# Performance work log

Measured on AMD Instinct MI355X. Metric: run time of the kernel, lower is better.

## Reference

```python
import jax, jax.numpy as jnp
import numpy as np

N_NODES = 100000
N_EDGES = 3200000
IN_DIM = 256
HIDDEN = 128
OUT_DIM = 64


def setup_inputs() -> dict:
    key = jax.random.key(0)
    k = jax.random.split(key, 6)
    x = jax.random.normal(k[0], (N_NODES, IN_DIM), dtype=jnp.float32)
    adj_vals = jax.random.uniform(k[1], (N_EDGES,), dtype=jnp.float32)
    # glorot init as in the original
    s1 = np.sqrt(6.0 / (IN_DIM + HIDDEN)).astype(np.float32)
    s2 = np.sqrt(6.0 / (HIDDEN + OUT_DIM)).astype(np.float32)
    w1 = jax.random.uniform(k[2], (IN_DIM, HIDDEN), dtype=jnp.float32, minval=-s1, maxval=s1)
    w2 = jax.random.uniform(k[3], (HIDDEN, OUT_DIM), dtype=jnp.float32, minval=-s2, maxval=s2)
    edge_src = jax.random.randint(k[4], (N_EDGES,), 0, N_NODES, dtype=jnp.int32)
    edge_dst = jax.random.randint(k[5], (N_EDGES,), 0, N_NODES, dtype=jnp.int32)
    return {"x": x, "adj_vals": adj_vals, "w1": w1, "w2": w2,
            "edge_src": edge_src, "edge_dst": edge_dst}


def _spmm(adj_vals, edge_src, edge_dst, h, n_nodes):
    """Sparse adjacency (COO) times dense matrix: out[d] = sum_e vals[e]*h[src[e]]."""
    msgs = adj_vals[:, None] * h[edge_src]  # [E, D] gather + scale
    return jax.ops.segment_sum(msgs, edge_dst, num_segments=n_nodes)


def reference(x, adj_vals, w1, w2, edge_src, edge_dst):
    # Layer 1: pre_sup = X @ W1; support = A @ pre_sup; relu
    h = jax.nn.relu(_spmm(adj_vals, edge_src, edge_dst, x @ w1, N_NODES))
    # Layer 2: identity activation -> logits
    logits = _spmm(adj_vals, edge_src, edge_dst, h @ w2, N_NODES)
    return logits
```

## Files before the change

kernel.cpp:

```cpp
#include <hip/hip_runtime.h>

#define N_NODES 100000
#define N_EDGES 3200000
#define IN_DIM 256
#define HIDDEN 128
#define OUT_DIM 64

#define NBUCK 782
#define CHUNK 2560
#define NPT (CHUNK / 256)
#define BCAP 6144
#define CURSTRIDE 32

typedef unsigned int uint32;
typedef unsigned short ushort16;

typedef short short8 __attribute__((ext_vector_type(8)));
typedef float f32x4 __attribute__((ext_vector_type(4)));

__device__ __forceinline__ ushort16 f2bf(float f) {
    uint32 u = __float_as_uint(f);
    u += 0x7fffu + ((u >> 16) & 1u);
    return (ushort16)(u >> 16);
}

__device__ __forceinline__ void splitbf(float f, unsigned short& hi, unsigned short& lo) {
    uint32 u = __float_as_uint(f);
    uint32 r = u + 0x7fffu + ((u >> 16) & 1u);
    hi = (unsigned short)(r >> 16);
    float hf = __uint_as_float((r >> 16) << 16);
    float res = f - hf;
    uint32 v = __float_as_uint(res);
    lo = (unsigned short)((v + 0x7fffu + ((v >> 16) & 1u)) >> 16);
}


__global__ __launch_bounds__(256)
void hist_bucket(const int* __restrict__ edst, int* __restrict__ bcnt, int E) {
    __shared__ int h[NBUCK];
    for (int b = threadIdx.x; b < NBUCK; b += 256) h[b] = 0;
    __syncthreads();
    for (int i = blockIdx.x * 256 + threadIdx.x; i < E; i += gridDim.x * 256)
        atomicAdd(&h[edst[i] >> 7], 1);
    __syncthreads();
    for (int b = threadIdx.x; b < NBUCK; b += 256) {
        int c = h[b];
        if (c) atomicAdd(&bcnt[b], c);
    }
}


__global__ __launch_bounds__(256)
void bucket_scan(const int* __restrict__ bcnt, int* __restrict__ bptr,
                 int* __restrict__ cursor, int* __restrict__ row_ptr, int E) {
    __shared__ int st[256];
    int tid = threadIdx.x;
    int v4[4];
    int s0 = 0;
#pragma unroll
    for (int k = 0; k < 4; k++) {
        int b = tid * 4 + k;
        v4[k] = (b < NBUCK) ? bcnt[b] : 0;
        s0 += v4[k];
    }
    st[tid] = s0;
    __syncthreads();
    for (int off = 1; off < 256; off <<= 1) {
        int t = (tid >= off) ? st[tid - off] : 0;
        __syncthreads();
        st[tid] += t;
        __syncthreads();
    }
    int run = st[tid] - s0;
#pragma unroll
    for (int k = 0; k < 4; k++) {
        int b = tid * 4 + k;
        if (b < NBUCK) { bptr[b] = run; cursor[b * CURSTRIDE] = run; }
        run += v4[k];
    }
    if (tid == 255) bptr[NBUCK] = run;
    if (tid == 0) row_ptr[N_NODES] = E;
}


__global__ __launch_bounds__(256)
void partition_kernel(const int* __restrict__ esrc, const int* __restrict__ edst,
                      const float* __restrict__ evals, int* __restrict__ cursor,
                      int2* __restrict__ part, int E) {
    __shared__ int hist[NBUCK];
    __shared__ int base_[NBUCK];
    int tid = threadIdx.x;
    long base = (long)blockIdx.x * CHUNK;
    int cnt = (int)min((long)CHUNK, (long)E - base);

    for (int b = tid; b < NBUCK; b += 256) hist[b] = 0;
    __syncthreads();

    int d[NPT];
#pragma unroll
    for (int k = 0; k < NPT; k++) {
        int j = tid + k * 256;
        d[k] = -1;
        if (j < cnt) {
            d[k] = edst[base + j];
            atomicAdd(&hist[d[k] >> 7], 1);
        }
    }
    __syncthreads();

    for (int b = tid; b < NBUCK; b += 256) {
        int c = hist[b];
        base_[b] = c ? atomicAdd(&cursor[b * CURSTRIDE], c) : 0;
        hist[b] = 0;
    }
    __syncthreads();

#pragma unroll
    for (int k = 0; k < NPT; k++) {
        int j = tid + k * 256;
        if (j < cnt) {
            int dd = d[k], b = dd >> 7;
            int off2 = atomicAdd(&hist[b], 1);
            part[base_[b] + off2] = make_int2(esrc[base + j] | ((dd & 127) << 17),
                                              __float_as_int(evals[base + j]));
        }
    }
}


__global__ __launch_bounds__(256)
void bucket_to_csr(const int* __restrict__ bptr, int2* __restrict__ part,
                   int* __restrict__ row_ptr) {
    __shared__ int2 se[BCAP];
    __shared__ int rcnt[128];
    __shared__ int rcur[128];
    int tid = threadIdx.x;
    int b = blockIdx.x;
    int s = bptr[b], e = bptr[b + 1];
    int cnt = min(e - s, BCAP);

    if (tid < 128) rcnt[tid] = 0;
    __syncthreads();
    for (int j = tid; j < cnt; j += 256) {
        int2 p = part[s + j];
        se[j] = p;
        atomicAdd(&rcnt[p.x >> 17], 1);
    }
    __syncthreads();

    int v = (tid < 128) ? rcnt[tid] : 0;
    if (tid < 128) rcur[tid] = v;
    __syncthreads();
    for (int off = 1; off < 128; off <<= 1) {
        int t = 0;
        if (tid < 128 && tid >= off) t = rcur[tid - off];
        __syncthreads();
        if (tid < 128 && tid >= off) rcur[tid] += t;
        __syncthreads();
    }
    if (tid < 128) {
        int excl = rcur[tid] - v;
        rcur[tid] = excl;
        int row = b * 128 + tid;
        if (row < N_NODES) row_ptr[row] = s + excl;
    }
    __syncthreads();

    for (int j = tid; j < cnt; j += 256) {
        int2 p = se[j];
        int r = p.x >> 17;
        int pos = atomicAdd(&rcur[r], 1);
        part[s + pos] = make_int2(p.x & 0x1FFFF, p.y);
    }
}


__global__ __launch_bounds__(256)
void splitw_kernel(const float* __restrict__ w1, const float* __restrict__ w2,
                   unsigned short* __restrict__ w1f_hi, unsigned short* __restrict__ w1f_lo,
                   unsigned short* __restrict__ w2f_hi, unsigned short* __restrict__ w2f_lo) {
    const int W1_SLOTS = (IN_DIM / 32) * (HIDDEN / 16) * 64;
    const int W2_SLOTS = (HIDDEN / 32) * (OUT_DIM / 16) * 64;
    int g = blockIdx.x * 256 + threadIdx.x;
    if (g < W1_SLOTS) {
        int lane = g & 63;
        int rest = g >> 6;
        int nfrag = rest & 7;
        int kblk = rest >> 3;
        int n = nfrag * 16 + (lane & 15);
        int k0 = kblk * 32 + (lane >> 4) * 8;
#pragma unroll
        for (int j = 0; j < 8; j++) {
            unsigned short h, l;
            splitbf(w1[(size_t)(k0 + j) * HIDDEN + n], h, l);
            w1f_hi[(size_t)g * 8 + j] = h;
            w1f_lo[(size_t)g * 8 + j] = l;
        }
    } else if (g < W1_SLOTS + W2_SLOTS) {
        int g2 = g - W1_SLOTS;
        int lane = g2 & 63;
        int rest = g2 >> 6;
        int nfrag = rest & 3;
        int kblk = rest >> 2;
        int n = nfrag * 16 + (lane & 15);
        int k0 = kblk * 32 + (lane >> 4) * 8;
#pragma unroll
        for (int j = 0; j < 8; j++) {
            unsigned short h, l;
            splitbf(w2[(size_t)(k0 + j) * OUT_DIM + n], h, l);
            w2f_hi[(size_t)g2 * 8 + j] = h;
            w2f_lo[(size_t)g2 * 8 + j] = l;
        }
    }
}


template <int K, int BN>
__launch_bounds__(256)
__global__ void gemm_mfma(const float* __restrict__ A,
                          const unsigned short* __restrict__ Bf_hi,
                          const unsigned short* __restrict__ Bf_lo,
                          ushort16* __restrict__ C, int M) {
    constexpr int BM = 128, BK = 64;
    constexpr int NF = BN / 32;
    __shared__ __align__(16) unsigned short Ah[BM * BK];
    __shared__ __align__(16) unsigned short Al[BM * BK];

    int tid = threadIdx.x;
    int wid = tid >> 6, lane = tid & 63;
    int wr = wid >> 1, wc = wid & 1;
    int rowBase = blockIdx.x * BM;
    int r = lane & 15, kg = lane >> 4;
    int swzmask = (lane & 7) << 4;

    f32x4 zero = {0.f, 0.f, 0.f, 0.f};
    f32x4 acc[4][NF];
#pragma unroll
    for (int m = 0; m < 4; m++)
#pragma unroll
        for (int n = 0; n < NF; n++) acc[m][n] = zero;

    int sk4 = (tid & 15) * 4;
    int sm0 = tid >> 4;

    for (int k0 = 0; k0 < K; k0 += BK) {
#pragma unroll
        for (int i = 0; i < 8; i++) {
            int m = sm0 + i * 16;
            int row = rowBase + m;
            float4 f = make_float4(0.f, 0.f, 0.f, 0.f);
            if (row < M) f = *(const float4*)(A + (size_t)row * K + k0 + sk4);
            ushort4 h, l;
            splitbf(f.x, h.x, l.x);
            splitbf(f.y, h.y, l.y);
            splitbf(f.z, h.z, l.z);
            splitbf(f.w, h.w, l.w);
            int bo = (m * BK + sk4) * 2;
            int swz = bo ^ ((m & 7) << 4);
            *(ushort4*)((char*)Ah + swz) = h;
            *(ushort4*)((char*)Al + swz) = l;
        }
        __syncthreads();

#pragma unroll
        for (int kk = 0; kk < BK / 32; kk++) {
            short8 ah[4], al[4];
            int abase = (wr * 64 + r) * (BK * 2) + kk * 64 + kg * 16;
#pragma unroll
            for (int m = 0; m < 4; m++) {
                int swz = (abase + m * (16 * BK * 2)) ^ swzmask;
                ah[m] = *(const short8*)((const char*)Ah + swz);
                al[m] = *(const short8*)((const char*)Al + swz);
            }
            short8 bh[NF], bl[NF];
            int kblk = (k0 >> 5) + kk;
#pragma unroll
            for (int n = 0; n < NF; n++) {
                int nf = wc * NF + n;
                size_t off = ((size_t)(kblk * (BN / 16) + nf) * 64 + lane) * 8;
                bh[n] = *(const short8*)(Bf_hi + off);
                bl[n] = *(const short8*)(Bf_lo + off);
            }
#pragma unroll
            for (int m = 0; m < 4; m++)
#pragma unroll
                for (int n = 0; n < NF; n++) {
                    acc[m][n] = __builtin_amdgcn_mfma_f32_16x16x32_bf16(ah[m], bh[n], acc[m][n], 0, 0, 0);
                    acc[m][n] = __builtin_amdgcn_mfma_f32_16x16x32_bf16(ah[m], bl[n], acc[m][n], 0, 0, 0);
                    acc[m][n] = __builtin_amdgcn_mfma_f32_16x16x32_bf16(al[m], bh[n], acc[m][n], 0, 0, 0);
                }
        }
        __syncthreads();
    }

#pragma unroll
    for (int m = 0; m < 4; m++) {
        int row0 = rowBase + wr * 64 + m * 16 + kg * 4;
#pragma unroll
        for (int j = 0; j < 4; j++) {
            int row = row0 + j;
            if (row < M) {
#pragma unroll
                for (int n = 0; n < NF; n++) {
                    int col = wc * (BN / 2) + n * 16 + r;
                    C[(size_t)row * BN + col] = f2bf(acc[m][n][j]);
                }
            }
        }
    }
}


template <int D, bool RELU>
__launch_bounds__(256)
__global__ void spmm_kernel(const ushort16* __restrict__ feat, const int2* __restrict__ csr_pair,
                            const int* __restrict__ row_ptr, float* __restrict__ out, int n) {
    constexpr int LPR = D * 2 / 16;
    constexpr int EPG = 64 / LPR;
    int wid = threadIdx.x >> 6;
    int lane = threadIdx.x & 63;
    int row = blockIdx.x * 4 + wid;
    if (row >= n) return;
    int s = row_ptr[row], e = row_ptr[row + 1];

    int sub = lane / LPR;
    int slot = lane % LPR;
    const char* fbase = (const char*)feat + slot * 16;

    float acc[8];
#pragma unroll
    for (int j = 0; j < 8; j++) acc[j] = 0.f;

    for (int i = s; i < e; i += 4 * EPG) {
        int2 p[4]; float v[4]; uint4 u[4];
#pragma unroll
        for (int q = 0; q < 4; q++) {
            int ii = i + q * EPG + sub;
            p[q] = csr_pair[min(ii, e - 1)];
            v[q] = (ii < e) ? __int_as_float(p[q].y) : 0.f;
        }
#pragma unroll
        for (int q = 0; q < 4; q++)
            u[q] = *(const uint4*)(fbase + (size_t)p[q].x * (D * 2));
#pragma unroll
        for (int q = 0; q < 4; q++) {
#pragma unroll
            for (int t = 0; t < 4; t++) {
                uint32 w = (&u[q].x)[t];
                acc[2 * t]     += v[q] * __uint_as_float(w << 16);
                acc[2 * t + 1] += v[q] * __uint_as_float(w & 0xffff0000u);
            }
        }
    }

#pragma unroll
    for (int m = LPR; m < 64; m <<= 1) {
#pragma unroll
        for (int j = 0; j < 8; j++) acc[j] += __shfl_xor(acc[j], m);
    }

    if (RELU) {
#pragma unroll
        for (int j = 0; j < 8; j++) acc[j] = acc[j] > 0.f ? acc[j] : 0.f;
    }

    if (lane < LPR) {
        float4* o = (float4*)(out + (size_t)row * D + slot * 8);
        o[0] = make_float4(acc[0], acc[1], acc[2], acc[3]);
        o[1] = make_float4(acc[4], acc[5], acc[6], acc[7]);
    }
}


extern "C" void kernel_launch(void* const* d_in, const int* in_sizes, int n_in,
                              void* d_out, int out_size, void* d_ws, size_t ws_size,
                              hipStream_t stream) {
    const float* x    = (const float*)d_in[0];
    const float* adj  = (const float*)d_in[1];
    const float* w1   = (const float*)d_in[2];
    const float* w2   = (const float*)d_in[3];
    const int*   esrc = (const int*)d_in[4];
    const int*   edst = (const int*)d_in[5];
    float* out = (float*)d_out;

    const int N = N_NODES;
    const int E = N_EDGES;

    char* ws = (char*)d_ws;
    size_t off = 0;
    auto take = [&](size_t bytes) -> char* {
        char* p = ws + off;
        off = (off + bytes + 255) & ~(size_t)255;
        return p;
    };
    int*      bcnt    = (int*)take((size_t)NBUCK * 4);
    int*      bptr    = (int*)take((size_t)(NBUCK + 1) * 4);
    int*      cursor  = (int*)take((size_t)NBUCK * CURSTRIDE * 4);
    int*      row_ptr = (int*)take((size_t)(N + 1) * 4);
    int2*     part    = (int2*)take((size_t)E * 8);
    ushort16* pre1    = (ushort16*)take((size_t)N * HIDDEN * 2);
    ushort16* pre2    = (ushort16*)take((size_t)N * OUT_DIM * 2);
    float*    h       = (float*)take((size_t)N * HIDDEN * 4);
    unsigned short* w1f_hi = (unsigned short*)take((size_t)HIDDEN * IN_DIM * 2);
    unsigned short* w1f_lo = (unsigned short*)take((size_t)HIDDEN * IN_DIM * 2);
    unsigned short* w2f_hi = (unsigned short*)take((size_t)OUT_DIM * HIDDEN * 2);
    unsigned short* w2f_lo = (unsigned short*)take((size_t)OUT_DIM * HIDDEN * 2);

    splitw_kernel<<<20, 256, 0, stream>>>(w1, w2, w1f_hi, w1f_lo, w2f_hi, w2f_lo);

    hipMemsetAsync(bcnt, 0, (size_t)NBUCK * 4, stream);
    hist_bucket<<<1024, 256, 0, stream>>>(edst, bcnt, E);
    bucket_scan<<<1, 256, 0, stream>>>(bcnt, bptr, cursor, row_ptr, E);
    partition_kernel<<<(E + CHUNK - 1) / CHUNK, 256, 0, stream>>>(esrc, edst, adj, cursor, part, E);
    bucket_to_csr<<<NBUCK, 256, 0, stream>>>(bptr, part, row_ptr);

    gemm_mfma<IN_DIM, HIDDEN><<<(N + 127) / 128, 256, 0, stream>>>(x, w1f_hi, w1f_lo, pre1, N);
    spmm_kernel<HIDDEN, true><<<(N + 3) / 4, 256, 0, stream>>>(pre1, part, row_ptr, h, N);

    gemm_mfma<HIDDEN, OUT_DIM><<<(N + 127) / 128, 256, 0, stream>>>(h, w2f_hi, w2f_lo, pre2, N);
    spmm_kernel<OUT_DIM, false><<<(N + 3) / 4, 256, 0, stream>>>(pre2, part, row_ptr, out, N);
}
```

Before: 547.7 us.

## Fuse edge partitioning with first GEMM and stage partition writes in LDS

Merges the edge partition kernel and the first X@W1 MFMA GEMM into one launch, with block index picking the role, so the two independent phases can overlap on the GPU. The partition path now sorts each chunk's edges by bucket in shared memory using a per-block prefix scan, then writes them out contiguously for more coalesced global stores. The chunk size is raised to fit this. This costs extra LDS per block (40KB), which may lower occupancy for the GEMM blocks, and adds a scan step.

```diff
diff --git a/kernel.cpp b/kernel.cpp
--- a/kernel.cpp
+++ b/kernel.cpp
@@ -7,8 +7,9 @@
 #define OUT_DIM 64
 
 #define NBUCK 782
-#define CHUNK 2560
+#define CHUNK 3072
 #define NPT (CHUNK / 256)
+#define NPB ((N_EDGES + CHUNK - 1) / CHUNK)
 #define BCAP 6144
 #define CURSTRIDE 32
 
@@ -80,51 +81,6 @@
     }
     if (tid == 255) bptr[NBUCK] = run;
     if (tid == 0) row_ptr[N_NODES] = E;
-}
-
-
-__global__ __launch_bounds__(256)
-void partition_kernel(const int* __restrict__ esrc, const int* __restrict__ edst,
-                      const float* __restrict__ evals, int* __restrict__ cursor,
-                      int2* __restrict__ part, int E) {
-    __shared__ int hist[NBUCK];
-    __shared__ int base_[NBUCK];
-    int tid = threadIdx.x;
-    long base = (long)blockIdx.x * CHUNK;
-    int cnt = (int)min((long)CHUNK, (long)E - base);
-
-    for (int b = tid; b < NBUCK; b += 256) hist[b] = 0;
-    __syncthreads();
-
-    int d[NPT];
-#pragma unroll
-    for (int k = 0; k < NPT; k++) {
-        int j = tid + k * 256;
-        d[k] = -1;
-        if (j < cnt) {
-            d[k] = edst[base + j];
-            atomicAdd(&hist[d[k] >> 7], 1);
-        }
-    }
-    __syncthreads();
-
-    for (int b = tid; b < NBUCK; b += 256) {
-        int c = hist[b];
-        base_[b] = c ? atomicAdd(&cursor[b * CURSTRIDE], c) : 0;
-        hist[b] = 0;
-    }
-    __syncthreads();
-
-#pragma unroll
-    for (int k = 0; k < NPT; k++) {
-        int j = tid + k * 256;
-        if (j < cnt) {
-            int dd = d[k], b = dd >> 7;
-            int off2 = atomicAdd(&hist[b], 1);
-            part[base_[b] + off2] = make_int2(esrc[base + j] | ((dd & 127) << 17),
-                                              __float_as_int(evals[base + j]));
-        }
-    }
 }
 
 
@@ -216,20 +172,19 @@
 
 
 template <int K, int BN>
-__launch_bounds__(256)
-__global__ void gemm_mfma(const float* __restrict__ A,
-                          const unsigned short* __restrict__ Bf_hi,
-                          const unsigned short* __restrict__ Bf_lo,
-                          ushort16* __restrict__ C, int M) {
+__device__ __forceinline__ void gemm_body(int bx, char* smem, const float* __restrict__ A,
+                                          const unsigned short* __restrict__ Bf_hi,
+                                          const unsigned short* __restrict__ Bf_lo,
+                                          ushort16* __restrict__ C, int M) {
     constexpr int BM = 128, BK = 64;
     constexpr int NF = BN / 32;
-    __shared__ __align__(16) unsigned short Ah[BM * BK];
-    __shared__ __align__(16) unsigned short Al[BM * BK];
+    unsigned short* Ah = (unsigned short*)smem;
+    unsigned short* Al = (unsigned short*)(smem + BM * BK * 2);
 
     int tid = threadIdx.x;
     int wid = tid >> 6, lane = tid & 63;
     int wr = wid >> 1, wc = wid & 1;
-    int rowBase = blockIdx.x * BM;
+    int rowBase = bx * BM;
     int r = lane & 15, kg = lane >> 4;
     int swzmask = (lane & 7) << 4;
 
@@ -308,6 +263,106 @@
             }
         }
     }
+}
+
+template <int K, int BN>
+__launch_bounds__(256)
+__global__ void gemm_mfma(const float* __restrict__ A,
+                          const unsigned short* __restrict__ Bf_hi,
+                          const unsigned short* __restrict__ Bf_lo,
+                          ushort16* __restrict__ C, int M) {
+    __shared__ __align__(16) char smem[32768];
+    gemm_body<K, BN>(blockIdx.x, smem, A, Bf_hi, Bf_lo, C, M);
+}
+
+
+__launch_bounds__(256)
+__global__ void partition_gemm1(const int* __restrict__ esrc, const int* __restrict__ edst,
+                                const float* __restrict__ evals, int* __restrict__ cursor,
+                                int2* __restrict__ part, int E,
+                                const float* __restrict__ A,
+                                const unsigned short* __restrict__ w1f_hi,
+                                const unsigned short* __restrict__ w1f_lo,
+                                ushort16* __restrict__ pre1, int M) {
+    __shared__ __align__(16) char smem[40960];
+    if (blockIdx.x >= NPB) {
+        gemm_body<IN_DIM, HIDDEN>(blockIdx.x - NPB, smem, A, w1f_hi, w1f_lo, pre1, M);
+        return;
+    }
+    int2* sbp  = (int2*)smem;
+    unsigned short* sbb = (unsigned short*)(smem + 24576);
+    int* hist  = (int*)(smem + 30720);
+    int* lst   = (int*)(smem + 33848);
+    int* bpos  = (int*)(smem + 36976);
+
+    int tid = threadIdx.x;
+    long base = (long)blockIdx.x * CHUNK;
+    int cnt = (int)min((long)CHUNK, (long)E - base);
+
+    for (int b = tid; b < NBUCK; b += 256) hist[b] = 0;
+    __syncthreads();
+
+    int d[NPT], sv[NPT]; float vv[NPT];
+#pragma unroll
+    for (int k = 0; k < NPT; k++) {
+        int j = tid + k * 256;
+        d[k] = -1;
+        if (j < cnt) {
+            d[k]  = edst[base + j];
+            sv[k] = esrc[base + j];
+            vv[k] = evals[base + j];
+            atomicAdd(&hist[d[k] >> 7], 1);
+        }
+    }
+    __syncthreads();
+
+    if (tid < 64) {
+        int c[13];
+        int run = 0;
+#pragma unroll
+        for (int k = 0; k < 13; k++) {
+            int b = tid * 13 + k;
+            c[k] = (b < NBUCK) ? hist[b] : 0;
+            run += c[k];
+        }
+        int sum = run;
+#pragma unroll
+        for (int off = 1; off < 64; off <<= 1) {
+            int up = __shfl_up(sum, off);
+            if (tid >= off) sum += up;
+        }
+        int excl = sum - run;
+#pragma unroll
+        for (int k = 0; k < 13; k++) {
+            int b = tid * 13 + k;
+            if (b < NBUCK) lst[b] = excl;
+            excl += c[k];
+        }
+    }
+    __syncthreads();
+
+    for (int b = tid; b < NBUCK; b += 256) {
+        int c = hist[b];
+        int g = c ? atomicAdd(&cursor[b * CURSTRIDE], c) : 0;
+        bpos[b] = g - lst[b];
+        hist[b] = lst[b];
+    }
+    __syncthreads();
+
+#pragma unroll
+    for (int k = 0; k < NPT; k++) {
+        int j = tid + k * 256;
+        if (j < cnt) {
+            int dd = d[k], b = dd >> 7;
+            int pos = atomicAdd(&hist[b], 1);
+            sbb[pos] = (unsigned short)b;
+            sbp[pos] = make_int2(sv[k] | ((dd & 127) << 17), __float_as_int(vv[k]));
+        }
+    }
+    __syncthreads();
+
+    for (int j = tid; j < cnt; j += 256)
+        part[bpos[sbb[j]] + j] = sbp[j];
 }
 
 
@@ -411,10 +466,12 @@
     hipMemsetAsync(bcnt, 0, (size_t)NBUCK * 4, stream);
     hist_bucket<<<1024, 256, 0, stream>>>(edst, bcnt, E);
     bucket_scan<<<1, 256, 0, stream>>>(bcnt, bptr, cursor, row_ptr, E);
-    partition_kernel<<<(E + CHUNK - 1) / CHUNK, 256, 0, stream>>>(esrc, edst, adj, cursor, part, E);
+
+    partition_gemm1<<<NPB + (N_NODES + 127) / 128, 256, 0, stream>>>(
+        esrc, edst, adj, cursor, part, E, x, w1f_hi, w1f_lo, pre1, N);
+
     bucket_to_csr<<<NBUCK, 256, 0, stream>>>(bptr, part, row_ptr);
 
-    gemm_mfma<IN_DIM, HIDDEN><<<(N + 127) / 128, 256, 0, stream>>>(x, w1f_hi, w1f_lo, pre1, N);
     spmm_kernel<HIDDEN, true><<<(N + 3) / 4, 256, 0, stream>>>(pre1, part, row_ptr, h, N);
 
     gemm_mfma<HIDDEN, OUT_DIM><<<(N + 127) / 128, 256, 0, stream>>>(h, w2f_hi, w2f_lo, pre2, N);
```

Measured after the change: 501.7 us. -8.4%, faster.
